# Kernel tuning notes

Measured on AMD Instinct MI355X. Metric: run time of the kernel, lower is better.

## Reference

```python
import jax, jax.numpy as jnp
import numpy as np

N, D_TOK, K = 8192, 256, 16


def knn_idx(xyz, k):
    # squared pairwise distances, diagonal excluded (loop=False)
    sq = jnp.sum(xyz * xyz, axis=-1)                      # [N]
    dist = sq[:, None] - 2.0 * (xyz @ xyz.T) + sq[None, :]  # [N,N]
    dist = dist + jnp.eye(xyz.shape[0], dtype=xyz.dtype) * jnp.asarray(1e10, xyz.dtype)
    _, idx = jax.lax.top_k(-dist, k)                      # [N,k] nearest neighbors j for each target i
    return idx


def edgeconv(x, nbr, W1, b1, W2, b2):
    # EdgeConv message: nn(concat(x_i, x_j - x_i)), aggr = max over neighbors
    n, d = x.shape
    k = nbr.shape[1]
    xi = x[:, None, :]                                    # [N,1,D]
    xj = x[nbr]                                           # [N,k,D] gather
    msg = jnp.concatenate([jnp.broadcast_to(xi, (n, k, d)), xj - xi], axis=-1)  # [N,k,2D]
    h = jax.nn.relu(msg @ W1 + b1) @ W2 + b2              # [N,k,token_dim]
    return jnp.max(h, axis=1)                             # [N,token_dim]


def setup_inputs() -> dict:
    key = jax.random.key(0)
    ks = jax.random.split(key, 10)
    d_in = 2 * (D_TOK + 3)
    s1 = 1.0 / np.sqrt(d_in)
    s2 = 1.0 / np.sqrt(D_TOK)
    return {
        "xyz": jax.random.normal(ks[0], (N, 3), dtype=jnp.float32),
        "feat": jax.random.normal(ks[1], (N, D_TOK), dtype=jnp.float32),
        "W1a": jax.random.normal(ks[2], (d_in, D_TOK), dtype=jnp.float32) * s1,
        "b1a": jnp.zeros((D_TOK,), dtype=jnp.float32),
        "W2a": jax.random.normal(ks[3], (D_TOK, D_TOK), dtype=jnp.float32) * s2,
        "b2a": jnp.zeros((D_TOK,), dtype=jnp.float32),
        "W1b": jax.random.normal(ks[4], (d_in, D_TOK), dtype=jnp.float32) * s1,
        "b1b": jnp.zeros((D_TOK,), dtype=jnp.float32),
        "W2b": jax.random.normal(ks[5], (D_TOK, D_TOK), dtype=jnp.float32) * s2,
        "b2b": jnp.zeros((D_TOK,), dtype=jnp.float32),
    }


def reference(xyz, feat, W1a, b1a, W2a, b2a, W1b, b1b, W2b, b2b):
    nbr = knn_idx(xyz, K)                                 # [N,k], built once, reused by both convs
    x = jnp.concatenate([feat, xyz], axis=-1)             # [N, D_TOK+3]
    x = edgeconv(x, nbr, W1a, b1a, W2a, b2a)              # [N, D_TOK]
    x = jnp.concatenate([x, xyz], axis=-1)                # [N, D_TOK+3]
    x = edgeconv(x, nbr, W1b, b1b, W2b, b2b)              # [N, D_TOK]
    return x
```

## Files before the change

kernel.cpp:

```cpp
#include <hip/hip_runtime.h>
#include <cfloat>

#define N_PTS 8192
#define DTOK 256
#define KNN 16

typedef __attribute__((ext_vector_type(8))) short short8;
typedef __attribute__((ext_vector_type(4))) float float4v;

__device__ inline short f2bf(float f) {
  unsigned u = __float_as_uint(f);
  u += 0x7fffu + ((u >> 16) & 1u);
  return (short)(u >> 16);
}
__device__ inline float bf2f(short h) {
  return __uint_as_float(((unsigned)(unsigned short)h) << 16);
}

__global__ __launch_bounds__(256) void knn_prep_kernel(
    const float* __restrict__ xyz, float4* __restrict__ xyz4) {
  const int i = blockIdx.x * 256 + threadIdx.x;
  float x = xyz[3 * i], y = xyz[3 * i + 1], z = xyz[3 * i + 2];
  float sq = __fadd_rn(__fadd_rn(__fmul_rn(x, x), __fmul_rn(y, y)),
                       __fmul_rn(z, z));
  xyz4[i] = make_float4(x, y, z, sq);
}

__global__ __launch_bounds__(256) void knn_select_kernel(
    const float4* __restrict__ xyz4, int* __restrict__ nbr) {
  const int lane = threadIdx.x & 63;
  const int i = blockIdx.x * 4 + (threadIdx.x >> 6);

  const float4 pi = xyz4[i];
  const float xi = pi.x, yi = pi.y, zi = pi.z, sqi = pi.w;

  float sd = FLT_MAX;
  int sj = 0;
  float s15 = FLT_MAX;

  for (int base = 0; base < N_PTS; base += 64) {
    const int j = base + lane;
    const float4 p = xyz4[j];
    const float dot = fmaf(zi, p.z, fmaf(yi, p.y, __fmul_rn(xi, p.x)));
    float d = __fadd_rn(__fsub_rn(sqi, __fmul_rn(2.0f, dot)), p.w);
    if (j == i) d = __fadd_rn(d, 1e10f);

    unsigned long long m = __ballot(d < s15);
    while (m) {
      const int src = __ffsll(m) - 1;
      m &= m - 1;
      const float dc = __shfl(d, src);
      if (dc < s15) {
        const int jc = base + src;
        const unsigned long long bm = __ballot(sd <= dc) & 0xFFFFull;
        const int pos = (int)__popcll(bm);
        const float pu = __shfl_up(sd, 1);
        const int ju = __shfl_up(sj, 1);
        if (lane < 16) {
          if (lane > pos)        { sd = pu; sj = ju; }
          else if (lane == pos)  { sd = dc; sj = jc; }
        }
        s15 = __shfl(sd, 15);
      }
    }
  }
  if (lane < 16) nbr[i * KNN + lane] = sj;
}

__global__ __launch_bounds__(256) void convert_w_kernel(
    const float* __restrict__ W1, short* __restrict__ bhi,
    short* __restrict__ blo) {
  const int n = blockIdx.x;
  const int k = threadIdx.x;
  const float v = (n < 256) ? W1[k * DTOK + n]
                            : W1[(259 + k) * DTOK + (n - 256)];
  short h = f2bf(v);
  bhi[n * 256 + k] = h;
  blo[n * 256 + k] = f2bf(v - bf2f(h));
}

__global__ __launch_bounds__(256, 2) void pq_gemm_fused_kernel(
    const float* __restrict__ A, const short* __restrict__ Bthi,
    const short* __restrict__ Btlo, const float* __restrict__ xyz,
    const float* __restrict__ W1, const float* __restrict__ b1,
    float* __restrict__ R, float* __restrict__ Q) {
  __shared__ short Ahi[64][32], Alo[64][32];
  __shared__ short Bhi[128][32], Blo[128][32];
  __shared__ float Qs[64][65];
  __shared__ float sx[64][3];
  __shared__ float swz[6][64];
  __shared__ float sb1[64];

  const int tid = threadIdx.x;
  const int lane = tid & 63;
  const int wave = tid >> 6;
  const int l15 = lane & 15;
  const int quad = lane >> 4;
  const int mh = wave & 1;
  const int qh = wave >> 1;
  const int m0 = blockIdx.x * 64;
  const int np0 = blockIdx.y * 64;

  if (tid < 64) {
    sx[tid][0] = xyz[(m0 + tid) * 3];
    sx[tid][1] = xyz[(m0 + tid) * 3 + 1];
    sx[tid][2] = xyz[(m0 + tid) * 3 + 2];
  } else if (tid < 128) {
    int n = tid - 64;
    sb1[n] = b1[np0 + n];
    #pragma unroll
    for (int r = 0; r < 3; ++r) {
      swz[r][n] = W1[(256 + r) * DTOK + np0 + n];
      swz[3 + r][n] = W1[(515 + r) * DTOK + np0 + n];
    }
  }

  float4v acc[2][4];
  #pragma unroll
  for (int mf = 0; mf < 2; ++mf)
    #pragma unroll
    for (int nf = 0; nf < 4; ++nf)
      #pragma unroll
      for (int e = 0; e < 4; ++e) acc[mf][nf][e] = 0.f;

  const int ar = tid >> 2;
  const int ak = (tid & 3) * 8;

  #pragma unroll 1
  for (int kc = 0; kc < 8; ++kc) {
    const int k0 = kc * 32;
    __syncthreads();
    {
      const float* asrc = A + (size_t)(m0 + ar) * 256 + k0 + ak;
      float4 a0 = *(const float4*)asrc;
      float4 a1 = *(const float4*)(asrc + 4);
      float v[8] = {a0.x, a0.y, a0.z, a0.w, a1.x, a1.y, a1.z, a1.w};
      short8 h8, l8;
      #pragma unroll
      for (int e = 0; e < 8; ++e) {
        short h = f2bf(v[e]);
        h8[e] = h;
        l8[e] = f2bf(v[e] - bf2f(h));
      }
      *(short8*)(&Ahi[ar][ak]) = h8;
      *(short8*)(&Alo[ar][ak]) = l8;
    }
    #pragma unroll
    for (int l = 0; l < 4; ++l) {
      const int rem = tid + 256 * (l & 1);
      const int row = rem >> 2;
      const int koff = (rem & 3) * 8;
      const int n = (row < 64) ? (np0 + row) : (256 + np0 + row - 64);
      const short* src = ((l < 2) ? Bthi : Btlo) + (size_t)n * 256 + k0 + koff;
      short8 vv = *(const short8*)src;
      if (l < 2) *(short8*)(&Bhi[row][koff]) = vv;
      else       *(short8*)(&Blo[row][koff]) = vv;
    }
    __syncthreads();

    short8 ah[2], al[2], bh[4], bl[4];
    #pragma unroll
    for (int mf = 0; mf < 2; ++mf) {
      ah[mf] = *(const short8*)(&Ahi[mh * 32 + mf * 16 + l15][quad * 8]);
      al[mf] = *(const short8*)(&Alo[mh * 32 + mf * 16 + l15][quad * 8]);
    }
    #pragma unroll
    for (int nf = 0; nf < 4; ++nf) {
      bh[nf] = *(const short8*)(&Bhi[qh * 64 + nf * 16 + l15][quad * 8]);
      bl[nf] = *(const short8*)(&Blo[qh * 64 + nf * 16 + l15][quad * 8]);
    }
    #pragma unroll
    for (int mf = 0; mf < 2; ++mf)
      #pragma unroll
      for (int nf = 0; nf < 4; ++nf) {
        acc[mf][nf] = __builtin_amdgcn_mfma_f32_16x16x32_bf16(
            ah[mf], bh[nf], acc[mf][nf], 0, 0, 0);
        acc[mf][nf] = __builtin_amdgcn_mfma_f32_16x16x32_bf16(
            ah[mf], bl[nf], acc[mf][nf], 0, 0, 0);
        acc[mf][nf] = __builtin_amdgcn_mfma_f32_16x16x32_bf16(
            al[mf], bh[nf], acc[mf][nf], 0, 0, 0);
      }
  }

  if (qh == 1) {
    #pragma unroll
    for (int mf = 0; mf < 2; ++mf)
      #pragma unroll
      for (int nf = 0; nf < 4; ++nf)
        #pragma unroll
        for (int e = 0; e < 4; ++e) {
          int row = mh * 32 + mf * 16 + quad * 4 + e;
          int col = nf * 16 + l15;
          float q = acc[mf][nf][e] + sx[row][0] * swz[3][col] +
                    sx[row][1] * swz[4][col] + sx[row][2] * swz[5][col];
          Qs[row][col] = q;
          Q[(size_t)(m0 + row) * DTOK + np0 + col] = q;
        }
  }
  __syncthreads();
  if (qh == 0) {
    #pragma unroll
    for (int mf = 0; mf < 2; ++mf)
      #pragma unroll
      for (int nf = 0; nf < 4; ++nf)
        #pragma unroll
        for (int e = 0; e < 4; ++e) {
          int row = mh * 32 + mf * 16 + quad * 4 + e;
          int col = nf * 16 + l15;
          float p = acc[mf][nf][e] + sx[row][0] * swz[0][col] +
                    sx[row][1] * swz[1][col] + sx[row][2] * swz[2][col];
          R[(size_t)(m0 + row) * DTOK + np0 + col] =
              (p + sb1[col]) - Qs[row][col];
        }
  }
}

#define EP 8

__global__ __launch_bounds__(256, 2) void edge_mfma_kernel(
    const float* __restrict__ R, const float* __restrict__ Q,
    const int* __restrict__ nbr, const float* __restrict__ W2,
    const float* __restrict__ b2, float* __restrict__ out,
    int num_groups, int groups_per_block) {
  __shared__ short Hs[EP * KNN * DTOK];
  const int lane = threadIdx.x & 63;
  const int wave = threadIdx.x >> 6;
  const int l15 = lane & 15;
  const int quad = lane >> 4;

  short8 bfr[4][8];
  #pragma unroll
  for (int nt_i = 0; nt_i < 4; ++nt_i) {
    const int n = (wave * 4 + nt_i) * 16 + l15;
    #pragma unroll
    for (int kt = 0; kt < 8; ++kt) {
      short8 f;
      #pragma unroll
      for (int jj = 0; jj < 8; ++jj) {
        int k = kt * 32 + quad * 8 + jj;
        f[jj] = f2bf(W2[k * DTOK + n]);
      }
      bfr[nt_i][kt] = f;
    }
  }

  const int wc8 = lane >> 1;
  const int wsub = (lane & 1) * 4;

  for (int gi = 0; gi < groups_per_block; ++gi) {
    const int g = blockIdx.x + gi * gridDim.x;
    if (g >= num_groups) break;
    const int i0 = g * EP;

    {
      const int ia = i0 + wave * 2;
      const int jr0 = nbr[ia * KNN + l15];
      const int jr1 = nbr[(ia + 1) * KNN + l15];
      const float4 ri0 = ((const float4*)(R + (size_t)ia * DTOK))[lane];
      const float4 ri1 = ((const float4*)(R + (size_t)(ia + 1) * DTOK))[lane];
      #pragma unroll
      for (int pp = 0; pp < 2; ++pp) {
        const float4 ri = pp ? ri1 : ri0;
        const int jr = pp ? jr1 : jr0;
        #pragma unroll
        for (int k = 0; k < KNN; ++k) {
          const int j = __shfl(jr, k, 16);
          const float4 qj = ((const float4*)(Q + (size_t)j * DTOK))[lane];
          const int r = wave * 32 + pp * 16 + k;
          uint2 pk;
          pk.x = ((unsigned)(unsigned short)f2bf(fmaxf(ri.x + qj.x, 0.f))) |
                 (((unsigned)(unsigned short)f2bf(fmaxf(ri.y + qj.y, 0.f))) << 16);
          pk.y = ((unsigned)(unsigned short)f2bf(fmaxf(ri.z + qj.z, 0.f))) |
                 (((unsigned)(unsigned short)f2bf(fmaxf(ri.w + qj.w, 0.f))) << 16);
          *(uint2*)(&Hs[r * DTOK + ((wc8 ^ (r & 7)) << 3) + wsub]) = pk;
        }
      }
    }
    __syncthreads();

    #pragma unroll
    for (int mp = 0; mp < 4; ++mp) {
      float4v acc[2][4];
      #pragma unroll
      for (int mi = 0; mi < 2; ++mi)
        #pragma unroll
        for (int nt_i = 0; nt_i < 4; ++nt_i)
          #pragma unroll
          for (int e = 0; e < 4; ++e) acc[mi][nt_i][e] = 0.f;

      #pragma unroll
      for (int kt = 0; kt < 8; ++kt) {
        const int pc = ((kt * 4 + quad) ^ (l15 & 7)) << 3;
        const short8 a0 = *(const short8*)(
            &Hs[((mp * 2 + 0) * 16 + l15) * DTOK + pc]);
        const short8 a1 = *(const short8*)(
            &Hs[((mp * 2 + 1) * 16 + l15) * DTOK + pc]);
        #pragma unroll
        for (int nt_i = 0; nt_i < 4; ++nt_i) {
          acc[0][nt_i] = __builtin_amdgcn_mfma_f32_16x16x32_bf16(
              a0, bfr[nt_i][kt], acc[0][nt_i], 0, 0, 0);
          acc[1][nt_i] = __builtin_amdgcn_mfma_f32_16x16x32_bf16(
              a1, bfr[nt_i][kt], acc[1][nt_i], 0, 0, 0);
        }
      }

      #pragma unroll
      for (int mi = 0; mi < 2; ++mi) {
        #pragma unroll
        for (int nt_i = 0; nt_i < 4; ++nt_i) {
          float rm = fmaxf(fmaxf(acc[mi][nt_i][0], acc[mi][nt_i][1]),
                           fmaxf(acc[mi][nt_i][2], acc[mi][nt_i][3]));
          rm = fmaxf(rm, __shfl_xor(rm, 16, 64));
          rm = fmaxf(rm, __shfl_xor(rm, 32, 64));
          if (lane < 16) {
            const int i = i0 + mp * 2 + mi;
            const int n = (wave * 4 + nt_i) * 16 + lane;
            out[(size_t)i * DTOK + n] = rm + b2[n];
          }
        }
      }
    }
    __syncthreads();
  }
}

extern "C" void kernel_launch(void* const* d_in, const int* in_sizes, int n_in,
                              void* d_out, int out_size, void* d_ws,
                              size_t ws_size, hipStream_t stream) {
  const float* xyz = (const float*)d_in[0];
  const float* feat = (const float*)d_in[1];
  const float* W1a = (const float*)d_in[2];
  const float* b1a = (const float*)d_in[3];
  const float* W2a = (const float*)d_in[4];
  const float* b2a = (const float*)d_in[5];
  const float* W1b = (const float*)d_in[6];
  const float* b1b = (const float*)d_in[7];
  const float* W2b = (const float*)d_in[8];
  const float* b2b = (const float*)d_in[9];
  float* out = (float*)d_out;

  char* w = (char*)d_ws;
  const size_t SZ_NBR = (size_t)N_PTS * KNN * sizeof(int);
  const size_t MB = 1024 * 1024;
  int* nbr = (int*)w;
  char* w1 = w + SZ_NBR;
  float4* xyz4 = (float4*)w1;
  float* R = (float*)(w1 + 8 * MB);
  float* Q = (float*)(w + SZ_NBR + 16 * MB);
  short* Bthi = (short*)(w + SZ_NBR + 24 * MB);
  short* Btlo = Bthi + 512 * 256;
  float* bufC = out;

  knn_prep_kernel<<<N_PTS / 256, 256, 0, stream>>>(xyz, xyz4);
  knn_select_kernel<<<N_PTS / 4, 256, 0, stream>>>(xyz4, nbr);

  const int num_groups = N_PTS / EP;
  const int nblocks = 512;

  convert_w_kernel<<<512, 256, 0, stream>>>(W1a, Bthi, Btlo);
  pq_gemm_fused_kernel<<<dim3(N_PTS / 64, 4), 256, 0, stream>>>(
      feat, Bthi, Btlo, xyz, W1a, b1a, R, Q);
  edge_mfma_kernel<<<nblocks, 256, 0, stream>>>(R, Q, nbr, W2a, b2a, bufC,
                                                num_groups, 2);

  convert_w_kernel<<<512, 256, 0, stream>>>(W1b, Bthi, Btlo);
  pq_gemm_fused_kernel<<<dim3(N_PTS / 64, 4), 256, 0, stream>>>(
      bufC, Bthi, Btlo, xyz, W1b, b1b, R, Q);
  edge_mfma_kernel<<<nblocks, 256, 0, stream>>>(R, Q, nbr, W2b, b2b, out,
                                                num_groups, 2);
}
```

Before: 265.3 us.

## Replace brute-force kNN with uniform-grid spatial binning and ring search

The all-pairs kNN scan, which checks every query against all 8192 points, is replaced by a uniform 32^3 grid. Points are binned with atomic counts, a single-block prefix scan and a scatter into cell-sorted order. Each query wave then searches outward in cubic shells of cells and stops once the 16th-best distance falls inside the searched radius, which cuts the number of distance evaluations. In exchange it adds several small kernel launches, including a serial single-block scan, and wave underuse on sparse cells. The fixed grid extent of [-4.5, 4.5] assumes roughly normally distributed coordinates, and ties are now broken by index.

New measurement: 496.4 us. 87.1% more time.

```diff
diff --git a/kernel.cpp b/kernel.cpp
--- a/kernel.cpp
+++ b/kernel.cpp
@@ -4,6 +4,8 @@
 #define N_PTS 8192
 #define DTOK 256
 #define KNN 16
+#define G 32
+#define NCELL (G * G * G)
 
 typedef __attribute__((ext_vector_type(8))) short short8;
 typedef __attribute__((ext_vector_type(4))) float float4v;
@@ -26,44 +28,139 @@
   xyz4[i] = make_float4(x, y, z, sq);
 }
 
-__global__ __launch_bounds__(256) void knn_select_kernel(
-    const float4* __restrict__ xyz4, int* __restrict__ nbr) {
+__global__ __launch_bounds__(256) void zero_cnt_kernel(int* __restrict__ c) {
+  c[blockIdx.x * 256 + threadIdx.x] = 0;
+}
+
+__device__ inline int cell_of(float v) {
+  int c = (int)floorf((v + 4.5f) * ((float)G / 9.0f));
+  return min(G - 1, max(0, c));
+}
+
+__global__ __launch_bounds__(256) void cell_assign_kernel(
+    const float4* __restrict__ xyz4, int* __restrict__ cnt,
+    int* __restrict__ cid, int* __restrict__ rank) {
+  const int i = blockIdx.x * 256 + threadIdx.x;
+  const float4 p = xyz4[i];
+  const int c = (cell_of(p.x) * G + cell_of(p.y)) * G + cell_of(p.z);
+  cid[i] = c;
+  rank[i] = atomicAdd(&cnt[c], 1);
+}
+
+__global__ __launch_bounds__(1024) void scan_kernel(
+    const int* __restrict__ cnt, int* __restrict__ start) {
+  __shared__ int tmp[1024];
+  const int tid = threadIdx.x;
+  int carry = 0;
+  for (int c = 0; c < NCELL / 1024; ++c) {
+    const int v = cnt[c * 1024 + tid];
+    tmp[tid] = v;
+    __syncthreads();
+    #pragma unroll
+    for (int off = 1; off < 1024; off <<= 1) {
+      int a = (tid >= off) ? tmp[tid - off] : 0;
+      __syncthreads();
+      tmp[tid] += a;
+      __syncthreads();
+    }
+    start[c * 1024 + tid] = carry + tmp[tid] - v;
+    carry += tmp[1023];
+    __syncthreads();
+  }
+  if (tid == 0) start[NCELL] = carry;
+}
+
+__global__ __launch_bounds__(256) void scatter_kernel(
+    const float4* __restrict__ xyz4, const int* __restrict__ cid,
+    const int* __restrict__ rank, const int* __restrict__ start,
+    float4* __restrict__ sx4, int* __restrict__ sj) {
+  const int i = blockIdx.x * 256 + threadIdx.x;
+  const int pos = start[cid[i]] + rank[i];
+  sx4[pos] = xyz4[i];
+  sj[pos] = i;
+}
+
+__global__ __launch_bounds__(256) void knn_query_kernel(
+    const float4* __restrict__ xyz4, const float4* __restrict__ sx4,
+    const int* __restrict__ sjA, const int* __restrict__ startA,
+    int* __restrict__ nbr) {
   const int lane = threadIdx.x & 63;
   const int i = blockIdx.x * 4 + (threadIdx.x >> 6);
 
   const float4 pi = xyz4[i];
   const float xi = pi.x, yi = pi.y, zi = pi.z, sqi = pi.w;
+  const int cx = cell_of(xi), cy = cell_of(yi), cz = cell_of(zi);
+  const float H = 9.0f / (float)G;
 
   float sd = FLT_MAX;
   int sj = 0;
-  float s15 = FLT_MAX;
-
-  for (int base = 0; base < N_PTS; base += 64) {
-    const int j = base + lane;
-    const float4 p = xyz4[j];
-    const float dot = fmaf(zi, p.z, fmaf(yi, p.y, __fmul_rn(xi, p.x)));
-    float d = __fadd_rn(__fsub_rn(sqi, __fmul_rn(2.0f, dot)), p.w);
-    if (j == i) d = __fadd_rn(d, 1e10f);
-
-    unsigned long long m = __ballot(d < s15);
-    while (m) {
-      const int src = __ffsll(m) - 1;
-      m &= m - 1;
-      const float dc = __shfl(d, src);
-      if (dc < s15) {
-        const int jc = base + src;
-        const unsigned long long bm = __ballot(sd <= dc) & 0xFFFFull;
-        const int pos = (int)__popcll(bm);
-        const float pu = __shfl_up(sd, 1);
-        const int ju = __shfl_up(sj, 1);
-        if (lane < 16) {
-          if (lane > pos)        { sd = pu; sj = ju; }
-          else if (lane == pos)  { sd = dc; sj = jc; }
-        }
-        s15 = __shfl(sd, 15);
-      }
-    }
-  }
+  float s15d = FLT_MAX;
+  int s15j = 0;
+
+  auto run = [&](int rs, int re) {
+    for (int b = rs; b < re; b += 64) {
+      const int idx = b + lane;
+      const bool act = idx < re;
+      const int ic = act ? idx : re - 1;
+      const float4 p = sx4[ic];
+      int jo = act ? sjA[ic] : 0x7fffffff;
+      const float dot = fmaf(zi, p.z, fmaf(yi, p.y, __fmul_rn(xi, p.x)));
+      float d = __fadd_rn(__fsub_rn(sqi, __fmul_rn(2.0f, dot)), p.w);
+      if (jo == i) d = __fadd_rn(d, 1e10f);
+      if (!act) d = FLT_MAX;
+
+      unsigned long long m =
+          __ballot((d < s15d) || (d == s15d && jo < s15j));
+      while (m) {
+        const int src = __ffsll(m) - 1;
+        m &= m - 1;
+        const float dc = __shfl(d, src);
+        const int jc = __shfl(jo, src);
+        if (dc < s15d || (dc == s15d && jc < s15j)) {
+          const unsigned long long bm =
+              __ballot(sd < dc || (sd == dc && sj < jc)) & 0xFFFFull;
+          const int pos = (int)__popcll(bm);
+          const float pu = __shfl_up(sd, 1);
+          const int ju = __shfl_up(sj, 1);
+          if (lane < 16) {
+            if (lane > pos)       { sd = pu; sj = ju; }
+            else if (lane == pos) { sd = dc; sj = jc; }
+          }
+          s15d = __shfl(sd, 15);
+          s15j = __shfl(sj, 15);
+        }
+      }
+    }
+  };
+
+  for (int s = 0;; ++s) {
+    if (s == 0) {
+      const int c0 = (cx * G + cy) * G + cz;
+      run(startA[c0], startA[c0 + 1]);
+    } else {
+      const int xlo = max(0, cx - s), xhi = min(G - 1, cx + s);
+      const int ylo = max(0, cy - s), yhi = min(G - 1, cy + s);
+      for (int x = xlo; x <= xhi; ++x) {
+        const int mx = abs(x - cx);
+        for (int y = ylo; y <= yhi; ++y) {
+          const int m2 = max(mx, abs(y - cy));
+          const int base = (x * G + y) * G;
+          if (m2 == s) {
+            const int zlo = max(0, cz - s), zhi = min(G - 1, cz + s);
+            run(startA[base + zlo], startA[base + zhi + 1]);
+          } else {
+            int z = cz - s;
+            if (z >= 0) run(startA[base + z], startA[base + z + 1]);
+            z = cz + s;
+            if (z < G) run(startA[base + z], startA[base + z + 1]);
+          }
+        }
+      }
+    }
+    const float bnd = (float)s * H;
+    if (s15d <= bnd * bnd - 1e-3f || s >= G) break;
+  }
+
   if (lane < 16) nbr[i * KNN + lane] = sj;
 }
 
@@ -342,9 +439,16 @@
   char* w = (char*)d_ws;
   const size_t SZ_NBR = (size_t)N_PTS * KNN * sizeof(int);
   const size_t MB = 1024 * 1024;
+  const size_t KB = 1024;
   int* nbr = (int*)w;
   char* w1 = w + SZ_NBR;
   float4* xyz4 = (float4*)w1;
+  float4* sx4 = (float4*)(w1 + 256 * KB);
+  int* sj = (int*)(w1 + 512 * KB);
+  int* cid = (int*)(w1 + 1 * MB);
+  int* rank = (int*)(w1 + 1 * MB + 256 * KB);
+  int* cnt = (int*)(w1 + 1 * MB + 512 * KB);
+  int* start = (int*)(w1 + 2 * MB);
   float* R = (float*)(w1 + 8 * MB);
   float* Q = (float*)(w + SZ_NBR + 16 * MB);
   short* Bthi = (short*)(w + SZ_NBR + 24 * MB);
@@ -352,7 +456,12 @@
   float* bufC = out;
 
   knn_prep_kernel<<<N_PTS / 256, 256, 0, stream>>>(xyz, xyz4);
-  knn_select_kernel<<<N_PTS / 4, 256, 0, stream>>>(xyz4, nbr);
+  zero_cnt_kernel<<<NCELL / 256, 256, 0, stream>>>(cnt);
+  cell_assign_kernel<<<N_PTS / 256, 256, 0, stream>>>(xyz4, cnt, cid, rank);
+  scan_kernel<<<1, 1024, 0, stream>>>(cnt, start);
+  scatter_kernel<<<N_PTS / 256, 256, 0, stream>>>(xyz4, cid, rank, start,
+                                                  sx4, sj);
+  knn_query_kernel<<<N_PTS / 4, 256, 0, stream>>>(xyz4, sx4, sj, start, nbr);
 
   const int num_groups = N_PTS / EP;
   const int nblocks = 512;
```
